# Kernel tuning notes

Measured on AMD Instinct MI355X. Metric: run time of the kernel, lower is better.

## Reference

```python
import jax, jax.numpy as jnp
import numpy as np

DIM = 1024
HEADS = 16
DIM_HEAD = 64
INNER = HEADS * DIM_HEAD  # 1024
EPS = 1e-5


def layernorm(x, w, b):
    mu = jnp.mean(x, axis=-1, keepdims=True)
    var = jnp.mean(jnp.square(x - mu), axis=-1, keepdims=True)
    return (x - mu) * jax.lax.rsqrt(var + EPS) * w + b


def setup_inputs() -> dict:
    key = jax.random.key(0)
    ks = jax.random.split(key, 9)
    b, n1, n2 = 4, 4096, 256
    x = jax.random.normal(ks[0], (b, n1, DIM), dtype=jnp.float32)
    latents = jax.random.normal(ks[1], (b, n2, DIM), dtype=jnp.float32)
    shift = jax.random.normal(ks[2], (b, HEADS), dtype=jnp.float32)
    scale = jax.random.normal(ks[3], (b, HEADS), dtype=jnp.float32)
    s = 1.0 / np.sqrt(DIM)
    Wq = jax.random.normal(ks[4], (DIM, INNER), dtype=jnp.float32) * s
    Wkv = jax.random.normal(ks[5], (DIM, 2 * INNER), dtype=jnp.float32) * s
    Wout = jax.random.normal(ks[6], (INNER, DIM), dtype=jnp.float32) * (1.0 / np.sqrt(INNER))
    ln1_w = jnp.ones((DIM,), jnp.float32)
    ln1_b = jnp.zeros((DIM,), jnp.float32)
    ln2_w = jnp.ones((DIM,), jnp.float32)
    ln2_b = jnp.zeros((DIM,), jnp.float32)
    return {"x": x, "latents": latents, "shift": shift, "scale": scale,
            "ln1_w": ln1_w, "ln1_b": ln1_b, "ln2_w": ln2_w, "ln2_b": ln2_b,
            "Wq": Wq, "Wkv": Wkv, "Wout": Wout}


def reference(x, latents, shift, scale, ln1_w, ln1_b, ln2_w, ln2_b, Wq, Wkv, Wout):
    b = x.shape[0]
    xn = layernorm(x, ln1_w, ln1_b)            # (b, n1, D)
    ln = layernorm(latents, ln2_w, ln2_b)      # (b, n2, D)
    q = ln @ Wq                                 # (b, n2, inner)
    kv = xn @ Wkv                               # (b, n1, 2*inner)
    k, v = jnp.split(kv, 2, axis=-1)
    q = q.reshape(b, -1, HEADS, DIM_HEAD)
    k = k.reshape(b, -1, HEADS, DIM_HEAD)
    v = v.reshape(b, -1, HEADS, DIM_HEAD)
    # AdaLN-style per-head modulation on q
    q = q * (1.0 + scale[:, None, :, None]) + shift[:, None, :, None]
    # fp32 attention scores (already fp32 here)
    attn_scale = DIM_HEAD ** -0.5
    qk = jnp.einsum('bihd,bjhd->bhij', q.astype(jnp.float32), k.astype(jnp.float32)) * attn_scale
    attn = jax.nn.softmax(qk, axis=-1).astype(v.dtype)  # (b, h, n2, n1)
    out = jnp.einsum('bhij,bjhd->bihd', attn, v)         # (b, n2, h, dh)
    out = out.reshape(b, -1, INNER)
    return out @ Wout
```

## Files before the change

kernel.cpp:

```cpp
#include <hip/hip_runtime.h>

typedef __bf16 bf16;
typedef bf16 bf16x8 __attribute__((ext_vector_type(8)));
typedef bf16 bf16x4 __attribute__((ext_vector_type(4)));
typedef float f32x4 __attribute__((ext_vector_type(4)));

#define B_ 4
#define N1 4096
#define N2 256
#define DIM 1024
#define HEADS 16
#define DH 64
#define INNER 1024
#define ASPLIT 4
#define KEYS_PER_SPLIT (N1 / ASPLIT)
#define SPLIT_ELEMS (4 * 16 * 256 * 64)

typedef __attribute__((address_space(1))) const void gvoid_t;
typedef __attribute__((address_space(3))) void lvoid_t;
__device__ __forceinline__ void async16(const void* g, void* l) {
  __builtin_amdgcn_global_load_lds((gvoid_t*)g, (lvoid_t*)l, 16, 0, 0);
}

__global__ __launch_bounds__(256) void ln_kernel(const float* __restrict__ src,
                                                 const float* __restrict__ w,
                                                 const float* __restrict__ bb,
                                                 bf16* __restrict__ dst) {
  int wv = threadIdx.x >> 6, lane = threadIdx.x & 63;
  int row = blockIdx.x * 4 + wv;
  const float4* p = (const float4*)(src + (size_t)row * DIM);
  float4 v[4];
  for (int j = 0; j < 4; j++) v[j] = p[j * 64 + lane];
  float s = 0.f, sq = 0.f;
  for (int j = 0; j < 4; j++) {
    s += v[j].x + v[j].y + v[j].z + v[j].w;
    sq += v[j].x * v[j].x + v[j].y * v[j].y + v[j].z * v[j].z + v[j].w * v[j].w;
  }
  for (int off = 32; off; off >>= 1) {
    s += __shfl_xor(s, off, 64);
    sq += __shfl_xor(sq, off, 64);
  }
  float mu = s * (1.0f / DIM);
  float var = sq * (1.0f / DIM) - mu * mu;
  float r = rsqrtf(var + 1e-5f);
  for (int j = 0; j < 4; j++) {
    float4 wv4 = ((const float4*)w)[j * 64 + lane];
    float4 bv4 = ((const float4*)bb)[j * 64 + lane];
    bf16x4 o;
    o[0] = (bf16)((v[j].x - mu) * r * wv4.x + bv4.x);
    o[1] = (bf16)((v[j].y - mu) * r * wv4.y + bv4.y);
    o[2] = (bf16)((v[j].z - mu) * r * wv4.z + bv4.z);
    o[3] = (bf16)((v[j].w - mu) * r * wv4.w + bv4.w);
    *(bf16x4*)(dst + (size_t)row * DIM + (j * 64 + lane) * 4) = o;
  }
}

__global__ __launch_bounds__(256) void transpose_w_all(
    const float* __restrict__ Wq, const float* __restrict__ Wkv,
    const float* __restrict__ Wout, bf16* __restrict__ WqT,
    bf16* __restrict__ WkvT, bf16* __restrict__ WoutT) {
  __shared__ float tile[32][33];
  int t = blockIdx.x;
  const float* src;
  bf16* dst;
  int N;
  if (t < 1024) { src = Wq; dst = WqT; N = 1024; }
  else if (t < 3072) { t -= 1024; src = Wkv; dst = WkvT; N = 2048; }
  else { t -= 3072; src = Wout; dst = WoutT; N = 1024; }
  int ntiles = N >> 5;
  int n0 = (t % ntiles) * 32, k0 = (t / ntiles) * 32;
  int x = threadIdx.x, y = threadIdx.y;
  for (int j = 0; j < 4; j++)
    tile[y + 8 * j][x] = src[(size_t)(k0 + y + 8 * j) * N + n0 + x];
  __syncthreads();
  for (int j = 0; j < 4; j++)
    dst[(size_t)(n0 + y + 8 * j) * 1024 + k0 + x] = (bf16)tile[x][y + 8 * j];
}

template <int MODE>
__global__ __launch_bounds__(256) void gemm_bf16(
    const bf16* __restrict__ A, const bf16* __restrict__ Bt,
    void* __restrict__ Cout, void* __restrict__ Cout2, int M, int N, int K,
    const float* __restrict__ shiftp, const float* __restrict__ scalep) {
  __shared__ __align__(16) bf16 smem[128 * 64 * 2];
  bf16* As = smem;
  bf16* Bs = smem + 128 * 64;
  int tid = threadIdx.x;
  int lane = tid & 63, wv = tid >> 6;
  int wr = wv >> 1, wc = wv & 1;
  int quad = lane >> 4, lr = lane & 15;
  int m0 = blockIdx.y * 128, n0 = blockIdx.x * 128;
  f32x4 acc[4][4] = {};
  for (int kt = 0; kt < K; kt += 64) {
    __syncthreads();
    for (int j = 0; j < 4; j++) {
      int idx0 = j * 256 + wv * 64;
      int row = (idx0 >> 3) + (lane >> 3);
      int cb = (lane & 7) ^ (row & 7);
      async16(&A[(size_t)(m0 + row) * K + kt + cb * 8], &As[idx0 * 8]);
      async16(&Bt[(size_t)(n0 + row) * K + kt + cb * 8], &Bs[idx0 * 8]);
    }
    __syncthreads();
    for (int kk = 0; kk < 2; kk++) {
      bf16x8 af[4], bfr[4];
      for (int im = 0; im < 4; im++) {
        int row = wr * 64 + im * 16 + lr;
        af[im] = *(const bf16x8*)&As[row * 64 + ((quad + 4 * kk) ^ (row & 7)) * 8];
      }
      for (int in = 0; in < 4; in++) {
        int row = wc * 64 + in * 16 + lr;
        bfr[in] = *(const bf16x8*)&Bs[row * 64 + ((quad + 4 * kk) ^ (row & 7)) * 8];
      }
      for (int im = 0; im < 4; im++)
        for (int in = 0; in < 4; in++)
          acc[im][in] = __builtin_amdgcn_mfma_f32_16x16x32_bf16(
              af[im], bfr[in], acc[im][in], 0, 0, 0);
    }
  }

  if (MODE == 0 && n0 >= 1024) {
    bf16* Ct = smem;
    for (int pass = 0; pass < 2; pass++) {
      __syncthreads();
      for (int inL = 0; inL < 2; inL++) {
        int in = pass * 2 + inL;
        int cc = wc * 32 + inL * 16 + lr;
        for (int im = 0; im < 4; im++) {
          int rb = wr * 64 + im * 16 + quad * 4;
          bf16x4 pk;
          for (int r = 0; r < 4; r++) pk[r] = (bf16)acc[im][in][r];
          *(bf16x4*)&Ct[cc * 136 + rb] = pk;
        }
      }
      __syncthreads();
      for (int k2 = 0; k2 < 4; k2++) {
        int ci = k2 * 256 + tid;
        int cc = ci >> 4, ch = ci & 15;
        uint4 val = *(const uint4*)&Ct[cc * 136 + ch * 8];
        int gco = (cc >> 5) * 64 + pass * 32 + (cc & 31);
        int col = n0 - 1024 + gco;
        int bb2 = m0 >> 12;
        int key = (m0 & 4095) + ch * 8;
        *(uint4*)&((bf16*)Cout2)[((size_t)(bb2 * 1024 + col)) * 4096 + key] = val;
      }
    }
    return;
  }

  for (int im = 0; im < 4; im++)
    for (int in = 0; in < 4; in++) {
      int col = n0 + wc * 64 + in * 16 + lr;
      for (int r = 0; r < 4; r++) {
        int row = m0 + wr * 64 + im * 16 + quad * 4 + r;
        float v = acc[im][in][r];
        if (MODE == 0) {
          ((bf16*)Cout)[(size_t)row * 1024 + col] = (bf16)v;
        } else if (MODE == 1) {
          int bb = row >> 8, hh = col >> 6;
          float sc = scalep[bb * 16 + hh], sh = shiftp[bb * 16 + hh];
          ((bf16*)Cout)[(size_t)row * N + col] =
              (bf16)((v * (1.0f + sc) + sh) * 0.18033688011112042f);
        } else {
          ((float*)Cout)[(size_t)row * N + col] = v;
        }
      }
    }
}

__global__ __launch_bounds__(256) void attn_kernel(const bf16* __restrict__ q,
                                                   const bf16* __restrict__ kb,
                                                   const bf16* __restrict__ vt,
                                                   float* __restrict__ opA,
                                                   float* __restrict__ opB,
                                                   float* __restrict__ ml) {
  int b = blockIdx.z, h = blockIdx.y;
  int qt = blockIdx.x & 3, sp = blockIdx.x >> 2;
  int tid = threadIdx.x, lane = tid & 63, wv = tid >> 6;
  int quad = lane >> 4, lr = lane & 15;
  __shared__ __align__(16) bf16 Ks[64 * 64];
  __shared__ __align__(16) bf16 Vs[64 * 64];
  __shared__ __align__(16) bf16 QP[64 * 64];
  __shared__ float abuf[4][16];
  int q0 = qt * 64;

  const bf16* qg = q + (size_t)(b * N2 + q0) * INNER + h * DH;
  for (int j = 0; j < 2; j++) {
    int r0 = j * 32 + wv * 8;
    int r = r0 + (lane >> 3);
    async16(&qg[(size_t)r * INNER + ((lane & 7) ^ (r & 7)) * 8], &QP[r0 * 64]);
  }
  __syncthreads();
  bf16x8 aQ[2];
  {
    int row = wv * 16 + lr;
    for (int kk = 0; kk < 2; kk++)
      aQ[kk] = *(const bf16x8*)&QP[row * 64 + ((quad + 4 * kk) ^ (row & 7)) * 8];
  }
  float m_s = -1e30f, l_s = 0.0f;
  f32x4 oacc[4] = {};

  const bf16* kg = kb + (size_t)(b * N1) * 1024 + h * DH;
  const bf16* vg = vt + (size_t)((b * HEADS + h) * DH) * N1;
  bf16* Ps = QP + wv * 1024;

  for (int t = 0; t < KEYS_PER_SPLIT / 64; t++) {
    int key0 = sp * KEYS_PER_SPLIT + t * 64;
    __syncthreads();
    for (int j = 0; j < 2; j++) {
      int r0 = j * 32 + wv * 8;
      int r = r0 + (lane >> 3);
      int cs = ((lane & 7) ^ (r & 7)) * 8;
      async16(&kg[(size_t)(key0 + r) * 1024 + cs], &Ks[r0 * 64]);
      async16(&vg[(size_t)r * N1 + key0 + cs], &Vs[r0 * 64]);
    }
    __syncthreads();

    f32x4 s[4] = {};
    for (int kk = 0; kk < 2; kk++)
      for (int nt = 0; nt < 4; nt++) {
        int row = nt * 16 + lr;
        bf16x8 ak =
            *(const bf16x8*)&Ks[row * 64 + ((quad + 4 * kk) ^ (row & 7)) * 8];
        s[nt] = __builtin_amdgcn_mfma_f32_16x16x32_bf16(ak, aQ[kk], s[nt], 0, 0, 0);
      }

    float mx = s[0][0];
    for (int nt = 0; nt < 4; nt++)
      for (int r = 0; r < 4; r++) mx = fmaxf(mx, s[nt][r]);
    mx = fmaxf(mx, __shfl_xor(mx, 16, 64));
    mx = fmaxf(mx, __shfl_xor(mx, 32, 64));
    float mn = fmaxf(m_s, mx);
    float al = exp2f(m_s - mn);
    float p[4][4], sum = 0.0f;
    for (int nt = 0; nt < 4; nt++)
      for (int r = 0; r < 4; r++) {
        p[nt][r] = exp2f(s[nt][r] - mn);
        sum += p[nt][r];
      }
    sum += __shfl_xor(sum, 16, 64);
    sum += __shfl_xor(sum, 32, 64);
    l_s = l_s * al + sum;
    m_s = mn;
    if (quad == 0) abuf[wv][lr] = al;

    for (int nt = 0; nt < 4; nt++) {
      bf16x4 pk;
      for (int r = 0; r < 4; r++) pk[r] = (bf16)p[nt][r];
      *(bf16x4*)&Ps[lr * 64 + ((2 * nt + (quad >> 1)) ^ (lr & 7)) * 8 +
                    (quad & 1) * 4] = pk;
    }

    f32x4 a4 = *(const f32x4*)&abuf[wv][quad * 4];
    for (int in = 0; in < 4; in++)
      for (int r = 0; r < 4; r++) oacc[in][r] *= a4[r];

    bf16x8 aP[2];
    for (int kk = 0; kk < 2; kk++)
      aP[kk] = *(const bf16x8*)&Ps[lr * 64 + ((4 * kk + quad) ^ (lr & 7)) * 8];

    for (int kk = 0; kk < 2; kk++)
      for (int in = 0; in < 4; in++) {
        int row = in * 16 + lr;
        bf16x8 bv =
            *(const bf16x8*)&Vs[row * 64 + ((quad + 4 * kk) ^ (row & 7)) * 8];
        oacc[in] = __builtin_amdgcn_mfma_f32_16x16x32_bf16(aP[kk], bv, oacc[in], 0, 0, 0);
      }
  }

  float* ob = (sp < 2 ? opA : opB) + (size_t)(sp & 1) * SPLIT_ELEMS;
  size_t rbase = (size_t)(b * HEADS + h) * N2;
  for (int r = 0; r < 4; r++) {
    int qq = q0 + wv * 16 + quad * 4 + r;
    for (int in = 0; in < 4; in++)
      ob[(rbase + qq) * 64 + in * 16 + lr] = oacc[in][r];
  }
  if (quad == 0) {
    int qq = q0 + wv * 16 + lr;
    float* mlp = ml + ((size_t)sp * (4 * HEADS * N2) + rbase + qq) * 2;
    mlp[0] = m_s;
    mlp[1] = l_s;
  }
}

__global__ __launch_bounds__(256) void combine_kernel(const float* __restrict__ opA,
                                                      const float* __restrict__ opB,
                                                      const float* __restrict__ ml,
                                                      bf16* __restrict__ out) {
  int gid = blockIdx.x * 256 + threadIdx.x;
  int d = gid & 63;
  int rq = gid >> 6;
  int qq = rq & 255, bh = rq >> 8;
  int h = bh & 15, b = bh >> 4;
  float m[ASPLIT], l[ASPLIT];
  for (int s = 0; s < ASPLIT; s++) {
    const float* p = ml + ((size_t)s * (4 * HEADS * N2) + rq) * 2;
    m[s] = p[0];
    l[s] = p[1];
  }
  float M = fmaxf(fmaxf(m[0], m[1]), fmaxf(m[2], m[3]));
  float L = 0.0f, o = 0.0f;
  for (int s = 0; s < ASPLIT; s++) {
    float w = exp2f(m[s] - M);
    L += w * l[s];
    const float* op = (s < 2 ? opA : opB) + (size_t)(s & 1) * SPLIT_ELEMS;
    o += w * op[(size_t)rq * 64 + d];
  }
  out[((size_t)(b * N2 + qq)) * INNER + h * DH + d] = (bf16)(o / L);
}

extern "C" void kernel_launch(void* const* d_in, const int* in_sizes, int n_in,
                              void* d_out, int out_size, void* d_ws,
                              size_t ws_size, hipStream_t stream) {
  const float* x       = (const float*)d_in[0];
  const float* latents = (const float*)d_in[1];
  const float* shift   = (const float*)d_in[2];
  const float* scale   = (const float*)d_in[3];
  const float* ln1w    = (const float*)d_in[4];
  const float* ln1b    = (const float*)d_in[5];
  const float* ln2w    = (const float*)d_in[6];
  const float* ln2b    = (const float*)d_in[7];
  const float* Wq      = (const float*)d_in[8];
  const float* Wkv     = (const float*)d_in[9];
  const float* Wout    = (const float*)d_in[10];

  char* ws = (char*)d_ws;
  bf16*  xn    = (bf16*)(ws);
  float* opA   = (float*)(ws);
  bf16*  lnl   = (bf16*)(ws + 33554432);
  float* ml    = (float*)(ws + 33554432);
  bf16*  qb    = (bf16*)(ws + 35651584);
  bf16*  kb    = (bf16*)(ws + 37748736);
  float* opB   = (float*)(ws + 71303168);
  bf16*  vtb   = (bf16*)(ws + 104857600);
  bf16*  aob   = (bf16*)(ws + 138412032);
  bf16*  WqT   = (bf16*)(ws + 140509184);
  bf16*  WkvT  = (bf16*)(ws + 142606336);
  bf16*  WoutT = (bf16*)(ws + 146800640);

  transpose_w_all<<<4096, dim3(32, 8), 0, stream>>>(Wq, Wkv, Wout, WqT, WkvT,
                                                    WoutT);
  ln_kernel<<<4096, 256, 0, stream>>>(x, ln1w, ln1b, xn);
  ln_kernel<<<256, 256, 0, stream>>>(latents, ln2w, ln2b, lnl);

  gemm_bf16<0><<<dim3(16, 128), 256, 0, stream>>>(xn, WkvT, kb, vtb, 16384,
                                                  2048, 1024, nullptr, nullptr);
  gemm_bf16<1><<<dim3(8, 8), 256, 0, stream>>>(lnl, WqT, qb, nullptr, 1024,
                                               1024, 1024, shift, scale);
  attn_kernel<<<dim3(4 * ASPLIT, 16, 4), 256, 0, stream>>>(qb, kb, vtb, opA,
                                                           opB, ml);
  combine_kernel<<<16384, 256, 0, stream>>>(opA, opB, ml, aob);
  gemm_bf16<2><<<dim3(8, 8), 256, 0, stream>>>(aob, WoutT, d_out, nullptr,
                                               1024, 1024, 1024, nullptr, nullptr);
}
```

Before: 311.2 us.

## Fuse layernorms, add 64x64 GEMM for small matmuls, remap KV GEMM blocks

Merges the two layernorm launches into one kernel that dispatches on row index. Adds a 64x64-tile GEMM for the Q and output projections so these 1024x1024 problems launch 256 blocks instead of 64 and fill more compute units. Remaps block IDs in the KV GEMM so neighbouring blocks work on nearby M rows across N columns, for better L2 reuse. It also swaps the query-tile and split index order in the attention grid. The smaller tiles cost more loads per FLOP in exchange for more parallelism.

```diff
diff --git a/kernel.cpp b/kernel.cpp
--- a/kernel.cpp
+++ b/kernel.cpp
@@ -22,12 +22,18 @@
   __builtin_amdgcn_global_load_lds((gvoid_t*)g, (lvoid_t*)l, 16, 0, 0);
 }
 
-__global__ __launch_bounds__(256) void ln_kernel(const float* __restrict__ src,
-                                                 const float* __restrict__ w,
-                                                 const float* __restrict__ bb,
-                                                 bf16* __restrict__ dst) {
+__global__ __launch_bounds__(256) void ln_all(
+    const float* __restrict__ x, const float* __restrict__ latents,
+    const float* __restrict__ ln1w, const float* __restrict__ ln1b,
+    const float* __restrict__ ln2w, const float* __restrict__ ln2b,
+    bf16* __restrict__ xn, bf16* __restrict__ lnl) {
   int wv = threadIdx.x >> 6, lane = threadIdx.x & 63;
-  int row = blockIdx.x * 4 + wv;
+  int grow = blockIdx.x * 4 + wv;
+  const float *src, *w, *bb;
+  bf16* dst;
+  int row;
+  if (grow < 16384) { src = x; w = ln1w; bb = ln1b; dst = xn; row = grow; }
+  else { src = latents; w = ln2w; bb = ln2b; dst = lnl; row = grow - 16384; }
   const float4* p = (const float4*)(src + (size_t)row * DIM);
   float4 v[4];
   for (int j = 0; j < 4; j++) v[j] = p[j * 64 + lane];
@@ -77,11 +83,9 @@
     dst[(size_t)(n0 + y + 8 * j) * 1024 + k0 + x] = (bf16)tile[x][y + 8 * j];
 }
 
-template <int MODE>
-__global__ __launch_bounds__(256) void gemm_bf16(
+__global__ __launch_bounds__(256) void gemm_kv(
     const bf16* __restrict__ A, const bf16* __restrict__ Bt,
-    void* __restrict__ Cout, void* __restrict__ Cout2, int M, int N, int K,
-    const float* __restrict__ shiftp, const float* __restrict__ scalep) {
+    bf16* __restrict__ Cout, bf16* __restrict__ Cout2, int K) {
   __shared__ __align__(16) bf16 smem[128 * 64 * 2];
   bf16* As = smem;
   bf16* Bs = smem + 128 * 64;
@@ -89,7 +93,11 @@
   int lane = tid & 63, wv = tid >> 6;
   int wr = wv >> 1, wc = wv & 1;
   int quad = lane >> 4, lr = lane & 15;
-  int m0 = blockIdx.y * 128, n0 = blockIdx.x * 128;
+  int bid = blockIdx.y * 16 + blockIdx.x;
+  int c = bid & 7, g = bid >> 3;
+  int mi = g & 7, nb = (g >> 3) & 15, chunk = g >> 7;
+  int m0 = (chunk * 64 + mi * 8 + c) * 128;
+  int n0 = nb * 128;
   f32x4 acc[4][4] = {};
   for (int kt = 0; kt < K; kt += 64) {
     __syncthreads();
@@ -118,7 +126,7 @@
     }
   }
 
-  if (MODE == 0 && n0 >= 1024) {
+  if (n0 >= 1024) {
     bf16* Ct = smem;
     for (int pass = 0; pass < 2; pass++) {
       __syncthreads();
@@ -141,7 +149,7 @@
         int col = n0 - 1024 + gco;
         int bb2 = m0 >> 12;
         int key = (m0 & 4095) + ch * 8;
-        *(uint4*)&((bf16*)Cout2)[((size_t)(bb2 * 1024 + col)) * 4096 + key] = val;
+        *(uint4*)&Cout2[((size_t)(bb2 * 1024 + col)) * 4096 + key] = val;
       }
     }
     return;
@@ -152,10 +160,57 @@
       int col = n0 + wc * 64 + in * 16 + lr;
       for (int r = 0; r < 4; r++) {
         int row = m0 + wr * 64 + im * 16 + quad * 4 + r;
+        Cout[(size_t)row * 1024 + col] = (bf16)acc[im][in][r];
+      }
+    }
+}
+
+template <int MODE>
+__global__ __launch_bounds__(256) void gemm64(
+    const bf16* __restrict__ A, const bf16* __restrict__ Bt,
+    void* __restrict__ Cout, int K, int N,
+    const float* __restrict__ shiftp, const float* __restrict__ scalep) {
+  __shared__ __align__(16) bf16 As[64 * 64];
+  __shared__ __align__(16) bf16 Bs[64 * 64];
+  int tid = threadIdx.x;
+  int lane = tid & 63, wv = tid >> 6;
+  int wr = wv >> 1, wc = wv & 1;
+  int quad = lane >> 4, lr = lane & 15;
+  int m0 = blockIdx.y * 64, n0 = blockIdx.x * 64;
+  f32x4 acc[2][2] = {};
+  for (int kt = 0; kt < K; kt += 64) {
+    __syncthreads();
+    for (int j = 0; j < 2; j++) {
+      int idx0 = j * 256 + wv * 64;
+      int row = (idx0 >> 3) + (lane >> 3);
+      int cb = (lane & 7) ^ (row & 7);
+      async16(&A[(size_t)(m0 + row) * K + kt + cb * 8], &As[idx0 * 8]);
+      async16(&Bt[(size_t)(n0 + row) * K + kt + cb * 8], &Bs[idx0 * 8]);
+    }
+    __syncthreads();
+    for (int kk = 0; kk < 2; kk++) {
+      bf16x8 af[2], bfr[2];
+      for (int im = 0; im < 2; im++) {
+        int row = wr * 32 + im * 16 + lr;
+        af[im] = *(const bf16x8*)&As[row * 64 + ((quad + 4 * kk) ^ (row & 7)) * 8];
+      }
+      for (int in = 0; in < 2; in++) {
+        int row = wc * 32 + in * 16 + lr;
+        bfr[in] = *(const bf16x8*)&Bs[row * 64 + ((quad + 4 * kk) ^ (row & 7)) * 8];
+      }
+      for (int im = 0; im < 2; im++)
+        for (int in = 0; in < 2; in++)
+          acc[im][in] = __builtin_amdgcn_mfma_f32_16x16x32_bf16(
+              af[im], bfr[in], acc[im][in], 0, 0, 0);
+    }
+  }
+  for (int im = 0; im < 2; im++)
+    for (int in = 0; in < 2; in++) {
+      int col = n0 + wc * 32 + in * 16 + lr;
+      for (int r = 0; r < 4; r++) {
+        int row = m0 + wr * 32 + im * 16 + quad * 4 + r;
         float v = acc[im][in][r];
-        if (MODE == 0) {
-          ((bf16*)Cout)[(size_t)row * 1024 + col] = (bf16)v;
-        } else if (MODE == 1) {
+        if (MODE == 1) {
           int bb = row >> 8, hh = col >> 6;
           float sc = scalep[bb * 16 + hh], sh = shiftp[bb * 16 + hh];
           ((bf16*)Cout)[(size_t)row * N + col] =
@@ -174,7 +229,7 @@
                                                    float* __restrict__ opB,
                                                    float* __restrict__ ml) {
   int b = blockIdx.z, h = blockIdx.y;
-  int qt = blockIdx.x & 3, sp = blockIdx.x >> 2;
+  int qt = blockIdx.x >> 2, sp = blockIdx.x & 3;
   int tid = threadIdx.x, lane = tid & 63, wv = tid >> 6;
   int quad = lane >> 4, lr = lane & 15;
   __shared__ __align__(16) bf16 Ks[64 * 64];
@@ -339,16 +394,14 @@
 
   transpose_w_all<<<4096, dim3(32, 8), 0, stream>>>(Wq, Wkv, Wout, WqT, WkvT,
                                                     WoutT);
-  ln_kernel<<<4096, 256, 0, stream>>>(x, ln1w, ln1b, xn);
-  ln_kernel<<<256, 256, 0, stream>>>(latents, ln2w, ln2b, lnl);
-
-  gemm_bf16<0><<<dim3(16, 128), 256, 0, stream>>>(xn, WkvT, kb, vtb, 16384,
-                                                  2048, 1024, nullptr, nullptr);
-  gemm_bf16<1><<<dim3(8, 8), 256, 0, stream>>>(lnl, WqT, qb, nullptr, 1024,
-                                               1024, 1024, shift, scale);
+  ln_all<<<4352, 256, 0, stream>>>(x, latents, ln1w, ln1b, ln2w, ln2b, xn, lnl);
+
+  gemm_kv<<<dim3(16, 128), 256, 0, stream>>>(xn, WkvT, kb, vtb, 1024);
+  gemm64<1><<<dim3(16, 16), 256, 0, stream>>>(lnl, WqT, qb, 1024, 1024, shift,
+                                              scale);
   attn_kernel<<<dim3(4 * ASPLIT, 16, 4), 256, 0, stream>>>(qb, kb, vtb, opA,
                                                            opB, ml);
   combine_kernel<<<16384, 256, 0, stream>>>(opA, opB, ml, aob);
-  gemm_bf16<2><<<dim3(8, 8), 256, 0, stream>>>(aob, WoutT, d_out, nullptr,
-                                               1024, 1024, 1024, nullptr, nullptr);
-}
+  gemm64<2><<<dim3(16, 16), 256, 0, stream>>>(aob, WoutT, d_out, 1024, 1024,
+                                              nullptr, nullptr);
+}
```

New measurement: 299.0 us. -3.9%, faster.
